# Kernel tuning notes

Measured on AMD Instinct MI355X. Metric: run time of the kernel, lower is better.

The kernel has to match this reference:

```python
import jax, jax.numpy as jnp
import numpy as np

B, L, D, H = 2, 2048, 1024, 16
DK = D // H


def setup_inputs() -> dict:
    key = jax.random.key(0)
    ks = jax.random.split(key, 11)
    s = 1.0 / np.sqrt(D)
    inp = {
        "context_sequence": jax.random.normal(ks[0], (B, L, D), jnp.float32),
        "value_sequence": jax.random.normal(ks[1], (B, L, D), jnp.float32),
        "mask": jnp.tril(jnp.ones((L, L), jnp.int32)),  # causal mask [L, L]
        "Wq": jax.random.normal(ks[2], (D, D), jnp.float32) * s,
        "bq": jax.random.normal(ks[3], (D,), jnp.float32) * s,
        "Wk": jax.random.normal(ks[4], (D, D), jnp.float32) * s,
        "bk": jax.random.normal(ks[5], (D,), jnp.float32) * s,
        "Wv": jax.random.normal(ks[6], (D, D), jnp.float32) * s,
        "bv": jax.random.normal(ks[7], (D,), jnp.float32) * s,
        "Wo": jax.random.normal(ks[8], (D, D), jnp.float32) * s,
        "bo": jax.random.normal(ks[9], (D,), jnp.float32) * s,
    }
    return inp


def reference(context_sequence, value_sequence, mask, Wq, bq, Wk, bk, Wv, bv, Wo, bo):
    orig_dtype = context_sequence.dtype
    # QKV projections; Q,K from context, V from value stream
    Q = (context_sequence @ Wq + bq).reshape(B, L, H, DK)
    K = (context_sequence @ Wk + bk).reshape(B, L, H, DK)
    V = (value_sequence @ Wv + bv).reshape(B, L, H, DK)
    # fp32 QK^T with 1/sqrt(d_k) scaling -> [B, H, L, L]
    scores = jnp.einsum("bqhd,bkhd->bhqk", Q.astype(jnp.float32), K.astype(jnp.float32)) / jnp.sqrt(
        jnp.asarray(DK, jnp.float32)
    )
    # dtype-dependent neg fill (fp32 -> -inf); causal rows always have >=1 valid entry
    neg_fill = jnp.asarray(-jnp.inf, jnp.float32)
    scores = jnp.where(mask[None, None, :, :] == 0, neg_fill, scores)
    scores = scores.astype(orig_dtype)
    attn = jax.nn.softmax(scores, axis=-1)
    # dropout is identity in eval mode
    out = jnp.einsum("bhqk,bkhd->bqhd", attn, V).reshape(B, L, D)
    return out @ Wo + bo
```

## Files before the change

kernel.cpp:

```cpp
#include <hip/hip_runtime.h>
#include <hip/hip_bf16.h>
#include <stdint.h>

#define B_   2
#define L_   2048
#define D_   1024
#define H_   16
#define DK_  64

typedef __attribute__((ext_vector_type(4))) float f32x4;
typedef __attribute__((ext_vector_type(8))) short short8;
typedef unsigned short ushort_t;

__device__ __forceinline__ ushort_t f2bf(float f) {
    union { float f; uint32_t u; } v; v.f = f;
    uint32_t r = v.u + 0x7FFFu + ((v.u >> 16) & 1u);
    return (ushort_t)(r >> 16);
}
__device__ __forceinline__ float bf2f(ushort_t u) {
    union { uint32_t u; float f; } v; v.u = (uint32_t)u << 16; return v.f;
}
__device__ __forceinline__ uint32_t pack_bf16_rne(float a, float b) {
    return (uint32_t)f2bf(a) | ((uint32_t)f2bf(b) << 16);
}

__device__ __forceinline__ void async_copy16(void* lds, const void* g) {
    __builtin_amdgcn_global_load_lds(
        (const __attribute__((address_space(1))) uint32_t*)g,
        (__attribute__((address_space(3))) uint32_t*)lds, 16, 0, 0);
}

__global__ void prep_kernel(const float* __restrict__ ctx, const float* __restrict__ val,
                            const float* __restrict__ w0, const float* __restrict__ w1,
                            const float* __restrict__ w2, const float* __restrict__ w3,
                            ushort_t* __restrict__ xc, ushort_t* __restrict__ xv,
                            ushort_t* __restrict__ wt) {
    __shared__ float tile[32][33];
    const int bid = blockIdx.x;
    if (bid < 8192) {
        const float* s = (bid >= 4096) ? val : ctx;
        ushort_t*    d = (bid >= 4096) ? xv : xc;
        int i = ((bid & 4095) * 256 + threadIdx.x) * 4;
        float4 v = *(const float4*)(s + i);
        ushort4 o;
        o.x = f2bf(v.x); o.y = f2bf(v.y); o.z = f2bf(v.z); o.w = f2bf(v.w);
        *(ushort4*)(d + i) = o;
    } else {
        const int t = bid - 8192;
        const int z = t >> 10;
        const int rem = t & 1023;
        const int by = rem >> 5, bx = rem & 31;
        const float* w = (z == 0) ? w0 : (z == 1) ? w1 : (z == 2) ? w2 : w3;
        ushort_t* o = wt + (size_t)z * D_ * D_;
        const int tx = threadIdx.x & 31, ty = threadIdx.x >> 5;
        const int k0 = by * 32, d0 = bx * 32;
#pragma unroll
        for (int i = 0; i < 4; i++)
            tile[ty + i * 8][tx] = w[(size_t)(k0 + ty + i * 8) * D_ + d0 + tx];
        __syncthreads();
#pragma unroll
        for (int i = 0; i < 4; i++)
            o[(size_t)(d0 + ty + i * 8) * D_ + k0 + tx] = f2bf(tile[tx][ty + i * 8]);
    }
}

template <bool SWAP>
__device__ __forceinline__ void gemm_main(const ushort_t* __restrict__ A,
                                          const ushort_t* __restrict__ WT,
                                          char* smem, int m0, int n0, int tid,
                                          f32x4 (&acc)[4][4]) {
    const int wid = tid >> 6, lane = tid & 63;
    const int wm = (wid >> 1) * 64, wn = (wid & 1) * 64;
#pragma unroll
    for (int i = 0; i < 4; i++)
#pragma unroll
        for (int j = 0; j < 4; j++) { f32x4 z = {0.f, 0.f, 0.f, 0.f}; acc[i][j] = z; }

    auto stage = [&](int buf, int k0) {
        char* bA = smem + buf * 32768;
        char* bB = bA + 16384;
#pragma unroll
        for (int i = 0; i < 4; i++) {
            int flat = i * 256 + tid; int row = flat >> 3; int win = (flat & 7) * 16;
            const char* srcA = (const char*)A + ((size_t)(m0 + row) * D_ + k0) * 2 + (win ^ ((row & 7) << 4));
            async_copy16(bA + (i * 256 + wid * 64) * 16, srcA);
            const char* srcB = (const char*)WT + ((size_t)(n0 + row) * D_ + k0) * 2 + (win ^ ((row & 7) << 4));
            async_copy16(bB + (i * 256 + wid * 64) * 16, srcB);
        }
    };

    stage(0, 0);
    int cur = 0;
    for (int k0 = 0; k0 < D_; k0 += 64) {
        __syncthreads();
        if (k0 + 64 < D_) stage(cur ^ 1, k0 + 64);
        const char* bA = smem + cur * 32768;
        const char* bB = bA + 16384;
#pragma unroll
        for (int ks = 0; ks < 2; ks++) {
            short8 af[4], bf[4];
            int kb = ks * 64 + ((lane >> 4) << 4);
#pragma unroll
            for (int t = 0; t < 4; t++) {
                int ml = wm + t * 16 + (lane & 15);
                af[t] = *(const short8*)(bA + ml * 128 + (kb ^ ((ml & 7) << 4)));
                int nl = wn + t * 16 + (lane & 15);
                bf[t] = *(const short8*)(bB + nl * 128 + (kb ^ ((nl & 7) << 4)));
            }
#pragma unroll
            for (int mt = 0; mt < 4; mt++)
#pragma unroll
                for (int nt = 0; nt < 4; nt++)
                    acc[mt][nt] = SWAP
                        ? __builtin_amdgcn_mfma_f32_16x16x32_bf16(bf[nt], af[mt], acc[mt][nt], 0, 0, 0)
                        : __builtin_amdgcn_mfma_f32_16x16x32_bf16(af[mt], bf[nt], acc[mt][nt], 0, 0, 0);
        }
        cur ^= 1;
    }
}

__device__ __forceinline__ void gemm_main8(const ushort_t* __restrict__ A,
                                           const ushort_t* __restrict__ WT,
                                           char* smem, int m0, int n0, int tid,
                                           f32x4 (&acc)[4][2]) {
    const int wid = tid >> 6, lane = tid & 63;
    const int wm = (wid >> 2) * 64, wn = (wid & 3) * 32;
#pragma unroll
    for (int i = 0; i < 4; i++)
#pragma unroll
        for (int j = 0; j < 2; j++) { f32x4 z = {0.f, 0.f, 0.f, 0.f}; acc[i][j] = z; }

    auto stage = [&](int buf, int k0) {
        char* bA = smem + buf * 32768;
        char* bB = bA + 16384;
#pragma unroll
        for (int i = 0; i < 2; i++) {
            int flat = i * 512 + tid; int row = flat >> 3; int win = (flat & 7) * 16;
            const char* srcA = (const char*)A + ((size_t)(m0 + row) * D_ + k0) * 2 + (win ^ ((row & 7) << 4));
            async_copy16(bA + (i * 512 + wid * 64) * 16, srcA);
            const char* srcB = (const char*)WT + ((size_t)(n0 + row) * D_ + k0) * 2 + (win ^ ((row & 7) << 4));
            async_copy16(bB + (i * 512 + wid * 64) * 16, srcB);
        }
    };

    stage(0, 0);
    int cur = 0;
    for (int k0 = 0; k0 < D_; k0 += 64) {
        __syncthreads();
        if (k0 + 64 < D_) stage(cur ^ 1, k0 + 64);
        const char* bA = smem + cur * 32768;
        const char* bB = bA + 16384;
#pragma unroll
        for (int ks = 0; ks < 2; ks++) {
            short8 af[4], bf[2];
            int kb = ks * 64 + ((lane >> 4) << 4);
#pragma unroll
            for (int t = 0; t < 4; t++) {
                int ml = wm + t * 16 + (lane & 15);
                af[t] = *(const short8*)(bA + ml * 128 + (kb ^ ((ml & 7) << 4)));
            }
#pragma unroll
            for (int t = 0; t < 2; t++) {
                int nl = wn + t * 16 + (lane & 15);
                bf[t] = *(const short8*)(bB + nl * 128 + (kb ^ ((nl & 7) << 4)));
            }
#pragma unroll
            for (int mt = 0; mt < 4; mt++)
#pragma unroll
                for (int nt = 0; nt < 2; nt++)
                    acc[mt][nt] = __builtin_amdgcn_mfma_f32_16x16x32_bf16(bf[nt], af[mt], acc[mt][nt], 0, 0, 0);
        }
        cur ^= 1;
    }
}

#define QSCALE 0.18033688f

__global__ __launch_bounds__(256, 2) void gemm_qkv(
    const ushort_t* __restrict__ Xc, const ushort_t* __restrict__ Xv,
    const ushort_t* __restrict__ WT0,
    const float* __restrict__ bq, const float* __restrict__ bk, const float* __restrict__ bv,
    ushort_t* __restrict__ qw, ushort_t* __restrict__ kw, ushort_t* __restrict__ vtw) {
    __shared__ __align__(16) char smem[65536];
    const int z = blockIdx.z;
    const ushort_t* A  = (z == 2) ? Xv : Xc;
    const ushort_t* WT = WT0 + (size_t)z * D_ * D_;
    const float* bias  = (z == 0) ? bq : (z == 1) ? bk : bv;
    const int tid = threadIdx.x, wid = tid >> 6, lane = tid & 63;
    const int lo = lane & 15, hi = lane >> 4;
    const int m0 = blockIdx.y * 128, n0 = blockIdx.x * 128;
    const int wm = (wid >> 1) * 64, wn = (wid & 1) * 64;
    f32x4 acc[4][4];
    if (z != 2) {
        gemm_main<true>(A, WT, smem, m0, n0, tid, acc);
#pragma unroll
        for (int mt = 0; mt < 4; mt++)
#pragma unroll
            for (int nt = 0; nt < 4; nt++) {
                int m  = m0 + wm + mt * 16 + lo;
                int nb = n0 + wn + nt * 16 + 4 * hi;
                float4 b4 = *(const float4*)(bias + nb);
                float v0 = acc[mt][nt][0] + b4.x;
                float v1 = acc[mt][nt][1] + b4.y;
                float v2 = acc[mt][nt][2] + b4.z;
                float v3 = acc[mt][nt][3] + b4.w;
                if (z == 0) { v0 *= QSCALE; v1 *= QSCALE; v2 *= QSCALE; v3 *= QSCALE; }
                int b = m >> 11, tok = m & 2047, h = nb >> 6, dk = nb & 63;
                uint2 w;
                w.x = pack_bf16_rne(v0, v1);
                w.y = pack_bf16_rne(v2, v3);
                ushort_t* outp = (z == 0) ? qw : kw;
                *(uint2*)(outp + ((size_t)(b * H_ + h) * L_ + tok) * DK_ + dk) = w;
            }
    } else {
        gemm_main<false>(A, WT, smem, m0, n0, tid, acc);
#pragma unroll
        for (int mt = 0; mt < 4; mt++)
#pragma unroll
            for (int nt = 0; nt < 4; nt++) {
                int n  = n0 + wn + nt * 16 + lo;
                int mb = m0 + wm + mt * 16 + 4 * hi;
                float bv_ = bias[n];
                int b = mb >> 11, tok = mb & 2047, h = n >> 6, dk = n & 63;
                uint2 w;
                w.x = pack_bf16_rne(acc[mt][nt][0] + bv_, acc[mt][nt][1] + bv_);
                w.y = pack_bf16_rne(acc[mt][nt][2] + bv_, acc[mt][nt][3] + bv_);
                *(uint2*)(vtw + ((size_t)(b * H_ + h) * DK_ + dk) * L_ + tok) = w;
            }
    }
}

__global__ __launch_bounds__(512, 2) void gemm_out(
    const ushort_t* __restrict__ O, const ushort_t* __restrict__ WT,
    const float* __restrict__ bo, float* __restrict__ out) {
    __shared__ __align__(16) char smem[65536];
    const int tid = threadIdx.x, wid = tid >> 6, lane = tid & 63;
    const int lo = lane & 15, hi = lane >> 4;
    const int m0 = blockIdx.y * 128, n0 = blockIdx.x * 128;
    const int wm = (wid >> 2) * 64, wn = (wid & 3) * 32;
    f32x4 acc[4][2];
    gemm_main8(O, WT, smem, m0, n0, tid, acc);
#pragma unroll
    for (int mt = 0; mt < 4; mt++)
#pragma unroll
        for (int nt = 0; nt < 2; nt++) {
            int m  = m0 + wm + mt * 16 + lo;
            int nb = n0 + wn + nt * 16 + 4 * hi;
            float4 b4 = *(const float4*)(bo + nb);
            float4 o;
            o.x = acc[mt][nt][0] + b4.x;
            o.y = acc[mt][nt][1] + b4.y;
            o.z = acc[mt][nt][2] + b4.z;
            o.w = acc[mt][nt][3] + b4.w;
            *(float4*)(out + (size_t)m * D_ + nb) = o;
        }
}

__global__ __launch_bounds__(256, 2) void attn_kernel(
    const ushort_t* __restrict__ qws, const ushort_t* __restrict__ kws,
    const ushort_t* __restrict__ vtws, ushort_t* __restrict__ ows) {
    __shared__ __align__(16) char smem[66560];
    const int tid = threadIdx.x, wid = tid >> 6, lane = tid & 63;
    const int lo = lane & 15, hi = lane >> 4;
    const int bid = blockIdx.x;
    const int xcd = bid & 7, slot = bid >> 3;
    const int bh = xcd * 4 + (slot >> 4);
    const int pi = slot & 15;
    char* P0 = smem + wid * 16384;
    char* P1 = P0 + 8192;
    float* lall = (float*)(smem + 65536);
    float* lw = lall + wid * 64;
    const int swz = (lo & 7) << 4;

    short8 ones;
#pragma unroll
    for (int i = 0; i < 8; i++) ones[i] = (short)0x3F80;
    const f32x4 minit = {-32.f, -32.f, -32.f, -32.f};

#pragma unroll 1
    for (int half = 0; half < 2; half++) {
        const int qtb = half ? (31 - pi) : pi;
        const int Q0 = qtb * 64;
        const int ntiles = qtb + 1;

        short8 qf[4][2];
#pragma unroll
        for (int qt = 0; qt < 4; qt++)
#pragma unroll
            for (int ks = 0; ks < 2; ks++)
                qf[qt][ks] = *(const short8*)(qws + (size_t)(bh * L_ + Q0 + qt * 16 + lo) * DK_ + ks * 32 + hi * 8);

        f32x4 oa[4][4];
        f32x4 lf4[4];
#pragma unroll
        for (int qt = 0; qt < 4; qt++) {
            f32x4 z = {0.f, 0.f, 0.f, 0.f};
            lf4[qt] = z;
#pragma unroll
            for (int ot = 0; ot < 4; ot++) oa[qt][ot] = z;
        }

        auto TILE = [&](int t, char* Pb) {
            const int k0 = t * 64;
            const bool diag = (t == qtb);
            short8 vf[4][2];
#pragma unroll
            for (int ot = 0; ot < 4; ot++)
#pragma unroll
                for (int ks = 0; ks < 2; ks++)
                    vf[ot][ks] = *(const short8*)(vtws + (size_t)(bh * DK_ + ot * 16 + lo) * L_ + k0 + ks * 32 + hi * 8);
#pragma unroll
            for (int kt = 0; kt < 4; kt++) {
                const ushort_t* krow = kws + (size_t)(bh * L_ + k0 + kt * 16 + lo) * DK_ + hi * 8;
                short8 kf0 = *(const short8*)(krow);
                short8 kf1 = *(const short8*)(krow + 32);
                const int kb = kt * 16 + 4 * hi;
#pragma unroll
                for (int qt = 0; qt < 4; qt++) {
                    f32x4 s = __builtin_amdgcn_mfma_f32_16x16x32_bf16(kf0, qf[qt][0], minit, 0, 0, 0);
                    s = __builtin_amdgcn_mfma_f32_16x16x32_bf16(kf1, qf[qt][1], s, 0, 0, 0);
                    float p0 = __builtin_amdgcn_exp2f(s[0]);
                    float p1 = __builtin_amdgcn_exp2f(s[1]);
                    float p2 = __builtin_amdgcn_exp2f(s[2]);
                    float p3 = __builtin_amdgcn_exp2f(s[3]);
                    if (diag) {
                        const int qg = qt * 16 + lo;
                        p0 = (kb > qg)     ? 0.f : p0;
                        p1 = (kb + 1 > qg) ? 0.f : p1;
                        p2 = (kb + 2 > qg) ? 0.f : p2;
                        p3 = (kb + 3 > qg) ? 0.f : p3;
                    }
                    uint2 w;
                    w.x = __builtin_amdgcn_perm(__float_as_uint(p1), __float_as_uint(p0), 0x07060302u);
                    w.y = __builtin_amdgcn_perm(__float_as_uint(p3), __float_as_uint(p2), 0x07060302u);
                    *(uint2*)(Pb + qt * 2048 + lo * 128 + ((kt * 32 + hi * 8) ^ swz)) = w;
                }
            }
            __builtin_amdgcn_s_setprio(1);
#pragma unroll
            for (int qt = 0; qt < 4; qt++)
#pragma unroll
                for (int ks = 0; ks < 2; ks++) {
                    short8 pf = *(const short8*)(Pb + qt * 2048 + lo * 128 + ((ks * 64 + hi * 16) ^ swz));
                    lf4[qt] = __builtin_amdgcn_mfma_f32_16x16x32_bf16(pf, ones, lf4[qt], 0, 0, 0);
#pragma unroll
                    for (int ot = 0; ot < 4; ot++)
                        oa[qt][ot] = __builtin_amdgcn_mfma_f32_16x16x32_bf16(pf, vf[ot][ks], oa[qt][ot], 0, 0, 0);
                }
            __builtin_amdgcn_s_setprio(0);
        };

        int t = wid;
#pragma unroll 1
        for (; t + 4 < ntiles; t += 8) {
            TILE(t, P0);
            TILE(t + 4, P1);
        }
        if (t < ntiles) TILE(t, P0);

#pragma unroll
        for (int qt = 0; qt < 4; qt++)
#pragma unroll
            for (int ot = 0; ot < 4; ot++)
#pragma unroll
                for (int r = 0; r < 4; r++)
                    *(ushort_t*)(P0 + (qt * 16 + 4 * hi + r) * 144 + (ot * 16 + lo) * 2) = f2bf(oa[qt][ot][r]);
        if (lo == 0) {
#pragma unroll
            for (int qt = 0; qt < 4; qt++)
                *(f32x4*)(lw + qt * 16 + 4 * hi) = lf4[qt];
        }
        __syncthreads();

        {
            const int q = tid >> 2, c = tid & 3;
            float acc[16];
#pragma unroll
            for (int j = 0; j < 16; j++) acc[j] = 0.f;
#pragma unroll
            for (int w = 0; w < 4; w++) {
                const char* base = smem + w * 16384 + q * 144 + c * 32;
                short8 a = *(const short8*)(base);
                short8 b = *(const short8*)(base + 16);
#pragma unroll
                for (int j = 0; j < 8; j++) acc[j]     += bf2f((ushort_t)a[j]);
#pragma unroll
                for (int j = 0; j < 8; j++) acc[8 + j] += bf2f((ushort_t)b[j]);
            }
            float ls = 0.f;
#pragma unroll
            for (int w = 0; w < 4; w++) ls += lall[w * 64 + q];
            float ri = 1.0f / ls;
            short8 o0, o1;
#pragma unroll
            for (int j = 0; j < 8; j++) o0[j] = (short)f2bf(acc[j] * ri);
#pragma unroll
            for (int j = 0; j < 8; j++) o1[j] = (short)f2bf(acc[8 + j] * ri);
            size_t ob = (size_t)((bh >> 4) * L_ + Q0 + q) * D_ + (bh & 15) * DK_ + c * 16;
            *(short8*)(ows + ob)     = o0;
            *(short8*)(ows + ob + 8) = o1;
        }
        __syncthreads();
    }
}

extern "C" void kernel_launch(void* const* d_in, const int* in_sizes, int n_in,
                              void* d_out, int out_size, void* d_ws, size_t ws_size,
                              hipStream_t stream) {
    (void)in_sizes; (void)n_in; (void)out_size; (void)ws_size;
    const float* ctx = (const float*)d_in[0];
    const float* val = (const float*)d_in[1];
    const float* Wq = (const float*)d_in[3];
    const float* bq = (const float*)d_in[4];
    const float* Wk = (const float*)d_in[5];
    const float* bk = (const float*)d_in[6];
    const float* Wv = (const float*)d_in[7];
    const float* bv = (const float*)d_in[8];
    const float* Wo = (const float*)d_in[9];
    const float* bo = (const float*)d_in[10];
    float* out = (float*)d_out;

    char* ws = (char*)d_ws;
    ushort_t* xc  = (ushort_t*)(ws);
    ushort_t* xv  = (ushort_t*)(ws + 8388608);
    ushort_t* wt  = (ushort_t*)(ws + 16777216);
    ushort_t* qws = (ushort_t*)(ws + 25165824);
    ushort_t* kws = (ushort_t*)(ws + 33554432);
    ushort_t* vtw = (ushort_t*)(ws + 41943040);

    prep_kernel<<<dim3(12288), 256, 0, stream>>>(ctx, val, Wq, Wk, Wv, Wo, xc, xv, wt);
    gemm_qkv<<<dim3(8, 32, 3), 256, 0, stream>>>(xc, xv, wt, bq, bk, bv, qws, kws, vtw);
    attn_kernel<<<dim3(512), 256, 0, stream>>>(qws, kws, vtw, xc );
    gemm_out<<<dim3(8, 32), 512, 0, stream>>>(xc, wt + (size_t)3 * D_ * D_, bo, out);
}
```

Measured before the change: 113.3 us.

## Split attention KV tiles across eight waves per block with swizzled reduction

After: 231.7 us. +104.5%, slower.

```diff
diff --git a/kernel.cpp b/kernel.cpp
--- a/kernel.cpp
+++ b/kernel.cpp
@@ -256,18 +256,17 @@
         }
 }
 
-__global__ __launch_bounds__(256, 2) void attn_kernel(
+__global__ __launch_bounds__(512, 4) void attn_kernel(
     const ushort_t* __restrict__ qws, const ushort_t* __restrict__ kws,
     const ushort_t* __restrict__ vtws, ushort_t* __restrict__ ows) {
-    __shared__ __align__(16) char smem[66560];
+    __shared__ __align__(16) char smem[67584];
     const int tid = threadIdx.x, wid = tid >> 6, lane = tid & 63;
     const int lo = lane & 15, hi = lane >> 4;
     const int bid = blockIdx.x;
     const int xcd = bid & 7, slot = bid >> 3;
     const int bh = xcd * 4 + (slot >> 4);
     const int pi = slot & 15;
-    char* P0 = smem + wid * 16384;
-    char* P1 = P0 + 8192;
+    char* P0 = smem + wid * 8192;
     float* lall = (float*)(smem + 65536);
     float* lw = lall + wid * 64;
     const int swz = (lo & 7) << 4;
@@ -300,7 +299,8 @@
             for (int ot = 0; ot < 4; ot++) oa[qt][ot] = z;
         }
 
-        auto TILE = [&](int t, char* Pb) {
+#pragma unroll 1
+        for (int t = wid; t < ntiles; t += 8) {
             const int k0 = t * 64;
             const bool diag = (t == qtb);
             short8 vf[4][2];
@@ -333,7 +333,7 @@
                     uint2 w;
                     w.x = __builtin_amdgcn_perm(__float_as_uint(p1), __float_as_uint(p0), 0x07060302u);
                     w.y = __builtin_amdgcn_perm(__float_as_uint(p3), __float_as_uint(p2), 0x07060302u);
-                    *(uint2*)(Pb + qt * 2048 + lo * 128 + ((kt * 32 + hi * 8) ^ swz)) = w;
+                    *(uint2*)(P0 + qt * 2048 + lo * 128 + ((kt * 32 + hi * 8) ^ swz)) = w;
                 }
             }
             __builtin_amdgcn_s_setprio(1);
@@ -341,30 +341,24 @@
             for (int qt = 0; qt < 4; qt++)
 #pragma unroll
                 for (int ks = 0; ks < 2; ks++) {
-                    short8 pf = *(const short8*)(Pb + qt * 2048 + lo * 128 + ((ks * 64 + hi * 16) ^ swz));
+                    short8 pf = *(const short8*)(P0 + qt * 2048 + lo * 128 + ((ks * 64 + hi * 16) ^ swz));
                     lf4[qt] = __builtin_amdgcn_mfma_f32_16x16x32_bf16(pf, ones, lf4[qt], 0, 0, 0);
 #pragma unroll
                     for (int ot = 0; ot < 4; ot++)
                         oa[qt][ot] = __builtin_amdgcn_mfma_f32_16x16x32_bf16(pf, vf[ot][ks], oa[qt][ot], 0, 0, 0);
                 }
             __builtin_amdgcn_s_setprio(0);
-        };
-
-        int t = wid;
-#pragma unroll 1
-        for (; t + 4 < ntiles; t += 8) {
-            TILE(t, P0);
-            TILE(t + 4, P1);
-        }
-        if (t < ntiles) TILE(t, P0);
+        }
 
 #pragma unroll
         for (int qt = 0; qt < 4; qt++)
 #pragma unroll
             for (int ot = 0; ot < 4; ot++)
 #pragma unroll
-                for (int r = 0; r < 4; r++)
-                    *(ushort_t*)(P0 + (qt * 16 + 4 * hi + r) * 144 + (ot * 16 + lo) * 2) = f2bf(oa[qt][ot][r]);
+                for (int r = 0; r < 4; r++) {
+                    int row = qt * 16 + 4 * hi + r;
+                    *(ushort_t*)(P0 + row * 128 + (((ot * 16 + lo) * 2) ^ ((row & 7) << 4))) = f2bf(oa[qt][ot][r]);
+                }
         if (lo == 0) {
 #pragma unroll
             for (int qt = 0; qt < 4; qt++)
@@ -373,32 +367,25 @@
         __syncthreads();
 
         {
-            const int q = tid >> 2, c = tid & 3;
-            float acc[16];
-#pragma unroll
-            for (int j = 0; j < 16; j++) acc[j] = 0.f;
-#pragma unroll
-            for (int w = 0; w < 4; w++) {
-                const char* base = smem + w * 16384 + q * 144 + c * 32;
-                short8 a = *(const short8*)(base);
-                short8 b = *(const short8*)(base + 16);
-#pragma unroll
-                for (int j = 0; j < 8; j++) acc[j]     += bf2f((ushort_t)a[j]);
-#pragma unroll
-                for (int j = 0; j < 8; j++) acc[8 + j] += bf2f((ushort_t)b[j]);
+            const int q = tid >> 3, c = tid & 7;
+            float acc[8];
+#pragma unroll
+            for (int e = 0; e < 8; e++) acc[e] = 0.f;
+#pragma unroll
+            for (int w = 0; w < 8; w++) {
+                short8 a = *(const short8*)(smem + w * 8192 + q * 128 + ((c * 16) ^ ((q & 7) << 4)));
+#pragma unroll
+                for (int e = 0; e < 8; e++) acc[e] += bf2f((ushort_t)a[e]);
             }
             float ls = 0.f;
 #pragma unroll
-            for (int w = 0; w < 4; w++) ls += lall[w * 64 + q];
+            for (int w = 0; w < 8; w++) ls += lall[w * 64 + q];
             float ri = 1.0f / ls;
-            short8 o0, o1;
-#pragma unroll
-            for (int j = 0; j < 8; j++) o0[j] = (short)f2bf(acc[j] * ri);
-#pragma unroll
-            for (int j = 0; j < 8; j++) o1[j] = (short)f2bf(acc[8 + j] * ri);
-            size_t ob = (size_t)((bh >> 4) * L_ + Q0 + q) * D_ + (bh & 15) * DK_ + c * 16;
-            *(short8*)(ows + ob)     = o0;
-            *(short8*)(ows + ob + 8) = o1;
+            short8 o;
+#pragma unroll
+            for (int e = 0; e < 8; e++) o[e] = (short)f2bf(acc[e] * ri);
+            size_t ob = (size_t)((bh >> 4) * L_ + Q0 + q) * D_ + (bh & 15) * DK_ + c * 8;
+            *(short8*)(ows + ob) = o;
         }
         __syncthreads();
     }
@@ -430,6 +417,6 @@
 
     prep_kernel<<<dim3(12288), 256, 0, stream>>>(ctx, val, Wq, Wk, Wv, Wo, xc, xv, wt);
     gemm_qkv<<<dim3(8, 32, 3), 256, 0, stream>>>(xc, xv, wt, bq, bk, bv, qws, kws, vtw);
-    attn_kernel<<<dim3(512), 256, 0, stream>>>(qws, kws, vtw, xc );
+    attn_kernel<<<dim3(512), 512, 0, stream>>>(qws, kws, vtw, xc );
     gemm_out<<<dim3(8, 32), 512, 0, stream>>>(xc, wt + (size_t)3 * D_ * D_, bo, out);
 }
```
